# Optimization experiments

Measured on AMD Instinct MI355X. Metric: run time of the kernel, lower is better.

The kernel has to match this reference:

```python
import jax, jax.numpy as jnp
import numpy as np

VOCAB, EMB, SEQ, HID, TAGS, BATCH = 50000, 300, 256, 256, 50, 128


def _lstm_relu(x, Wx, Wh, b, reverse):
    """Keras LSTM with activation='relu', recurrent_activation='sigmoid'.
    x: [B,S,E] -> returns hidden states [B,S,H]. Gate order i,f,g,o (Keras)."""
    B = x.shape[0]
    H = Wh.shape[0]
    # Precompute input projections for all timesteps: [S,B,4H]
    xz = jnp.einsum('bse,eg->sbg', x, Wx) + b

    def step(carry, z_t):
        h, c = carry
        z = z_t + h @ Wh
        i, f, g, o = jnp.split(z, 4, axis=-1)
        c = jax.nn.sigmoid(f) * c + jax.nn.sigmoid(i) * jax.nn.relu(g)
        h = jax.nn.sigmoid(o) * jax.nn.relu(c)
        return (h, c), h

    h0 = jnp.zeros((B, H), x.dtype)
    _, hs = jax.lax.scan(step, (h0, h0), xz, reverse=reverse)  # hs: [S,B,H] in time order
    return jnp.swapaxes(hs, 0, 1)  # [B,S,H]


def setup_inputs() -> dict:
    key = jax.random.key(0)
    ks = jax.random.split(key, 10)
    s = 0.05  # small init keeps relu-LSTM states numerically tame
    return {
        'tokens': jax.random.randint(ks[0], (BATCH, SEQ), 0, VOCAB, dtype=jnp.int32),
        'emb':    jax.random.normal(ks[1], (VOCAB, EMB), jnp.float32) * s,
        'Wx_f':   jax.random.normal(ks[2], (EMB, 4 * HID), jnp.float32) * s,
        'Wh_f':   jax.random.normal(ks[3], (HID, 4 * HID), jnp.float32) * s,
        'b_f':    jnp.zeros((4 * HID,), jnp.float32),
        'Wx_b':   jax.random.normal(ks[4], (EMB, 4 * HID), jnp.float32) * s,
        'Wh_b':   jax.random.normal(ks[5], (HID, 4 * HID), jnp.float32) * s,
        'b_b':    jnp.zeros((4 * HID,), jnp.float32),
        'Wd':     jax.random.normal(ks[6], (2 * HID, TAGS), jnp.float32) * s,
        'bd':     jnp.zeros((TAGS,), jnp.float32),
    }


def reference(tokens, emb, Wx_f, Wh_f, b_f, Wx_b, Wh_b, b_b, Wd, bd):
    x = emb[tokens]                                  # [B,S,E] embedding lookup
    hf = _lstm_relu(x, Wx_f, Wh_f, b_f, reverse=False)
    hb = _lstm_relu(x, Wx_b, Wh_b, b_b, reverse=True)
    h = jnp.concatenate([hf, hb], axis=-1)           # [B,S,2H]
    # Dropout is identity at inference (Keras default training=False).
    return jax.nn.softmax(h @ Wd + bd, axis=-1)      # [B,S,TAGS]
```

## Files before the change

kernel.cpp:

```cpp
#include <hip/hip_runtime.h>
#include <stdint.h>

#define B_    128
#define S_    256
#define EMB_  300
#define HID_  256
#define TAGS_ 50
#define KPAD  320
#define NROWS (B_ * S_)
#define GF    (4 * HID_)
#define NCOLS (2 * GF)

typedef __bf16 bf16x8 __attribute__((ext_vector_type(8)));
typedef float  f32x4  __attribute__((ext_vector_type(4)));
typedef unsigned int u32x4 __attribute__((ext_vector_type(4)));
typedef int    i32x8  __attribute__((ext_vector_type(8)));

__device__ __forceinline__ unsigned short f2bf(float f) {
    unsigned int u = __float_as_uint(f);
    unsigned int r = (u + 0x7fffu + ((u >> 16) & 1u)) >> 16;
    return (unsigned short)r;
}
__device__ __forceinline__ bf16x8 ldb8(const unsigned short* p) {
    u32x4 v = *reinterpret_cast<const u32x4*>(p);
    return __builtin_bit_cast(bf16x8, v);
}
__device__ __forceinline__ float sigf(float x) {
    return __builtin_amdgcn_rcpf(1.0f + __builtin_amdgcn_exp2f(x * -1.44269504f));
}
__device__ __forceinline__ float sel2(f32x4 v, int p) {
    return p ? v[1] : v[0];
}
__device__ __forceinline__ void gload_lds16(const void* g, void* l) {
    __builtin_amdgcn_global_load_lds(
        (const __attribute__((address_space(1))) void*)g,
        (__attribute__((address_space(3))) void*)l, 16, 0, 0);
}

__global__ void k_gather_x(const int* __restrict__ tokens, const float* __restrict__ emb,
                           unsigned short* __restrict__ X16) {
    int r = blockIdx.x;
    int k = threadIdx.x;
    int b = r & 127, s = r >> 7;
    int tok = tokens[b * S_ + s];
    float v = (k < EMB_) ? emb[(long)tok * EMB_ + k] : 0.0f;
    X16[(long)r * KPAD + k] = f2bf(v);
}

__global__ void k_prep_w(const float* __restrict__ Wx_f, const float* __restrict__ Wx_b,
                         unsigned short* __restrict__ W16T) {
    int c = blockIdx.x;
    int k = threadIdx.x;
    float v = 0.0f;
    if (k < EMB_) v = (c < GF) ? Wx_f[k * GF + c] : Wx_b[k * GF + (c - GF)];
    W16T[c * KPAD + k] = f2bf(v);
}

__global__ void k_prep_wd(const float* __restrict__ Wd, unsigned short* __restrict__ WdT16) {
    int c = blockIdx.x;
    int k = threadIdx.x;
    float v = (c < TAGS_) ? Wd[k * TAGS_ + c] : 0.0f;
    WdT16[c * 512 + k] = f2bf(v);
}

__global__ void k_prep_wh8(const float* __restrict__ Wh_f, const float* __restrict__ Wh_b,
                           unsigned char* __restrict__ WhP8) {
    int row = blockIdx.x;
    int k = threadIdx.x;
    int d = row >> 10, rr = row & 1023, gi = rr >> 8, j = rr & 255;
    const float* Wh = d ? Wh_b : Wh_f;
    float v = Wh[k * GF + gi * HID_ + j];
    int p = __builtin_amdgcn_cvt_pk_fp8_f32(v, 0.0f, 0, false);
    WhP8[(long)row * 256 + k] = (unsigned char)(p & 0xff);
}

__global__ __launch_bounds__(256) void k_gemm_xz(
    const unsigned short* __restrict__ X16, const unsigned short* __restrict__ W16T,
    const float* __restrict__ b_f, const float* __restrict__ b_b,
    unsigned long long* __restrict__ xzP) {
    __shared__ __align__(16) unsigned short Asw[2][128 * 64];
    __shared__ __align__(16) unsigned short Bsw[2][128 * 64];
    int w = threadIdx.x >> 6, lane = threadIdx.x & 63;
    int quad = lane >> 4, l16 = lane & 15;
    int m0 = blockIdx.x * 128;
    int n0 = blockIdx.y * 128;

    int rlane = lane >> 3;
    int jpos  = lane & 7;
    int jsrc  = jpos ^ (rlane & 7);

    f32x4 acc[2][8];
#pragma unroll
    for (int mt = 0; mt < 2; ++mt)
#pragma unroll
        for (int nt = 0; nt < 8; ++nt) acc[mt][nt] = (f32x4){0.f, 0.f, 0.f, 0.f};

#define STAGE(ST, BUFI) do {                                                    \
    int k0_ = (ST) * 64;                                                        \
    _Pragma("unroll")                                                           \
    for (int i_ = 0; i_ < 4; ++i_) {                                            \
        int rb_ = (w * 4 + i_) * 8;                                             \
        int r_  = rb_ + rlane;                                                  \
        gload_lds16(X16 + (long)(m0 + r_) * KPAD + k0_ + jsrc * 8,              \
                    &Asw[BUFI][rb_ * 64]);                                      \
    }                                                                           \
    _Pragma("unroll")                                                           \
    for (int i_ = 0; i_ < 4; ++i_) {                                            \
        int rb_ = (w * 4 + i_) * 8;                                             \
        int r_  = rb_ + rlane;                                                  \
        gload_lds16(W16T + (long)(n0 + r_) * KPAD + k0_ + jsrc * 8,             \
                    &Bsw[BUFI][rb_ * 64]);                                      \
    }                                                                           \
} while (0)

    STAGE(0, 0);
    __syncthreads();
#pragma unroll
    for (int st = 0; st < 5; ++st) {
        if (st < 4) STAGE(st + 1, (st + 1) & 1);
        int bufi = st & 1;
#pragma unroll
        for (int ks = 0; ks < 2; ++ks) {
            bf16x8 a[2], bb[8];
#pragma unroll
            for (int mt = 0; mt < 2; ++mt) {
                int mrow = w * 32 + mt * 16 + l16;
                int jp = (ks * 4 + quad) ^ (l16 & 7);
                a[mt] = ldb8(&Asw[bufi][mrow * 64 + jp * 8]);
            }
#pragma unroll
            for (int nt = 0; nt < 8; ++nt) {
                int nrow = nt * 16 + l16;
                int jp = (ks * 4 + quad) ^ (l16 & 7);
                bb[nt] = ldb8(&Bsw[bufi][nrow * 64 + jp * 8]);
            }
#pragma unroll
            for (int mt = 0; mt < 2; ++mt)
#pragma unroll
                for (int nt = 0; nt < 8; ++nt)
                    acc[mt][nt] = __builtin_amdgcn_mfma_f32_16x16x32_bf16(a[mt], bb[nt], acc[mt][nt], 0, 0, 0);
        }
        __syncthreads();
    }
#undef STAGE

    int s = blockIdx.x;
#pragma unroll
    for (int mt = 0; mt < 2; ++mt) {
        int grp = w * 2 + mt;
#pragma unroll
        for (int nt = 0; nt < 8; ++nt) {
            int col = n0 + nt * 16 + l16;
            int dir = col >> 10, cc = col & 1023;
            int gate = cc >> 8, u16 = (cc & 255) >> 4;
            float bias = dir ? b_b[cc] : b_f[cc];
            unsigned long long pk = 0;
#pragma unroll
            for (int r = 0; r < 4; ++r)
                pk |= (unsigned long long)f2bf(acc[mt][nt][r] + bias) << (16 * r);
            long idx8 = ((long)(s * 16 + dir * 8 + grp)) * 4096 +
                        (gate * 16 + u16) * 64 + quad * 16 + l16;
            xzP[idx8] = pk;
        }
    }
}

__global__ __launch_bounds__(512, 2) void k_recurrence(
    const unsigned char* __restrict__ WhP8,
    const unsigned long long* __restrict__ xzP, unsigned short* __restrict__ hcat16) {
    __shared__ __align__(16) unsigned char lds[1152];
    int tid = threadIdx.x;
    int w = tid >> 6, lane = tid & 63, quad = lane >> 4, l16 = lane & 15;
    int blk = blockIdx.x;
    int d = blk >> 6, bg2 = blk & 63;
    int p = quad & 1;
    int cg = quad >> 1;
    int col = 16 * (2 * w + cg) + l16;
    int rp = l16 & 1;

    i32x8 wh8s[4][2][2];
#pragma unroll
    for (int gi = 0; gi < 4; ++gi)
#pragma unroll
        for (int cgi = 0; cgi < 2; ++cgi)
#pragma unroll
            for (int kt2 = 0; kt2 < 2; ++kt2) {
                const unsigned char* wp8 = WhP8 +
                    ((long)((d * 4 + gi) * 256 + 16 * (2 * w + cgi) + l16)) * 256 +
                    kt2 * 128 + quad * 32;
                i32x8 v = *reinterpret_cast<const i32x8*>(wp8);
                asm volatile("" : "+v"(v));
                wh8s[gi][cgi][kt2] = v;
            }

    float c2 = 0.f;

    const unsigned short* xzU = (const unsigned short*)xzP;
    int rowc = d * 8 + (bg2 >> 3);
    unsigned int laneoff = (unsigned)((2 * w + cg) * 256 +
                                      (((bg2 >> 1) & 3) * 16 + l16) * 4 +
                                      2 * (bg2 & 1) + p);

    unsigned short xzu[4];
    {
        int s0 = d ? 255 : 0;
        const unsigned short* ps = xzU + (unsigned long)(s0 * 16 + rowc) * 16384;
#pragma unroll
        for (int ga = 0; ga < 4; ++ga) xzu[ga] = ps[laneoff + ga * 4096];
    }

    for (int t = 0; t < 256; ++t) {
        int s = d ? (255 - t) : t;
        int pb = t & 1, cb = pb ^ 1;
        f32x4 acc8[4][2];
#pragma unroll
        for (int gi = 0; gi < 4; ++gi)
#pragma unroll
            for (int cgi = 0; cgi < 2; ++cgi) acc8[gi][cgi] = (f32x4){0.f, 0.f, 0.f, 0.f};

        if (t > 0) {
#pragma unroll
            for (int kt2 = 0; kt2 < 2; ++kt2) {
                i32x8 A8 = *reinterpret_cast<const i32x8*>(
                    lds + cb * 576 + rp * 288 + kt2 * 128 + quad * 32);
#pragma unroll
                for (int cgi = 0; cgi < 2; ++cgi)
#pragma unroll
                    for (int gi = 0; gi < 4; ++gi)
#if __has_builtin(__builtin_amdgcn_mfma_scale_f32_16x16x128_f8f6f4)
                        acc8[gi][cgi] = __builtin_amdgcn_mfma_scale_f32_16x16x128_f8f6f4(
                            A8, wh8s[gi][cgi][kt2], acc8[gi][cgi], 0, 0, 0, 0x7F, 0, 0x7F);
#else
                        acc8[gi][cgi] = acc8[gi][cgi];
#endif
            }
        }
        float xa0 = __uint_as_float((unsigned int)xzu[0] << 16);
        float xa1 = __uint_as_float((unsigned int)xzu[1] << 16);
        float xa2 = __uint_as_float((unsigned int)xzu[2] << 16);
        float xa3 = __uint_as_float((unsigned int)xzu[3] << 16);
        {
            int sn = d ? (s ? s - 1 : 0) : (s < 255 ? s + 1 : 255);
            const unsigned short* ps = xzU + (unsigned long)(sn * 16 + rowc) * 16384;
#pragma unroll
            for (int ga = 0; ga < 4; ++ga) xzu[ga] = ps[laneoff + ga * 4096];
        }
        float zi = (cg ? sel2(acc8[0][1], p) : sel2(acc8[0][0], p)) + xa0;
        float zf = (cg ? sel2(acc8[1][1], p) : sel2(acc8[1][0], p)) + xa1;
        float zg = (cg ? sel2(acc8[2][1], p) : sel2(acc8[2][0], p)) + xa2;
        float zo = (cg ? sel2(acc8[3][1], p) : sel2(acc8[3][0], p)) + xa3;
        float c = sigf(zf) * c2 + sigf(zi) * fmaxf(zg, 0.0f);
        c2 = c;
        float h = sigf(zo) * fmaxf(c, 0.0f);

        int p8 = __builtin_amdgcn_cvt_pk_fp8_f32(h, h, 0, false);
        *(lds + pb * 576 + p * 288 + col) = (unsigned char)(p8 & 0xff);
        hcat16[((long)(bg2 * 2 + p) * S_ + s) * 512 + d * HID_ + col] = f2bf(h);
        asm volatile("s_waitcnt lgkmcnt(0)\n\ts_barrier" ::: "memory");
    }
}

__global__ __launch_bounds__(256) void k_gemm_logits(
    const unsigned short* __restrict__ hcat16, const unsigned short* __restrict__ WdT16,
    const float* __restrict__ bd, float* __restrict__ out) {
    int w = threadIdx.x >> 6, lane = threadIdx.x & 63;
    int quad = lane >> 4, l16 = lane & 15;
    int m0 = blockIdx.x * 128 + w * 32;
    f32x4 acc[2][4];
#pragma unroll
    for (int mt = 0; mt < 2; ++mt)
#pragma unroll
        for (int nt = 0; nt < 4; ++nt) acc[mt][nt] = (f32x4){0.f, 0.f, 0.f, 0.f};
#pragma unroll
    for (int ks = 0; ks < 16; ++ks) {
        int k0 = ks * 32 + quad * 8;
        bf16x8 a[2], bb[4];
#pragma unroll
        for (int mt = 0; mt < 2; ++mt)
            a[mt] = ldb8(hcat16 + (long)(m0 + mt * 16 + l16) * 512 + k0);
#pragma unroll
        for (int nt = 0; nt < 4; ++nt)
            bb[nt] = ldb8(WdT16 + (long)(nt * 16 + l16) * 512 + k0);
#pragma unroll
        for (int mt = 0; mt < 2; ++mt)
#pragma unroll
            for (int nt = 0; nt < 4; ++nt)
                acc[mt][nt] = __builtin_amdgcn_mfma_f32_16x16x32_bf16(a[mt], bb[nt], acc[mt][nt], 0, 0, 0);
    }
#pragma unroll
    for (int mt = 0; mt < 2; ++mt) {
#pragma unroll
        for (int r = 0; r < 4; ++r) {
            int row = m0 + mt * 16 + quad * 4 + r;
            float vv[4];
            float mx = -3.0e38f;
#pragma unroll
            for (int nt = 0; nt < 4; ++nt) {
                int cl = nt * 16 + l16;
                float tv = (cl < TAGS_) ? (acc[mt][nt][r] + bd[cl]) : -3.0e38f;
                vv[nt] = tv;
                mx = fmaxf(mx, tv);
            }
#pragma unroll
            for (int off = 8; off >= 1; off >>= 1) mx = fmaxf(mx, __shfl_xor(mx, off, 64));
            float sum = 0.f;
#pragma unroll
            for (int nt = 0; nt < 4; ++nt) {
                int cl = nt * 16 + l16;
                float e = (cl < TAGS_) ? __expf(vv[nt] - mx) : 0.0f;
                vv[nt] = e;
                sum += e;
            }
#pragma unroll
            for (int off = 8; off >= 1; off >>= 1) sum += __shfl_xor(sum, off, 64);
            float rs = __builtin_amdgcn_rcpf(sum);
#pragma unroll
            for (int nt = 0; nt < 4; ++nt) {
                int cl = nt * 16 + l16;
                if (cl < TAGS_) out[(long)row * TAGS_ + cl] = vv[nt] * rs;
            }
        }
    }
}

extern "C" void kernel_launch(void* const* d_in, const int* in_sizes, int n_in,
                              void* d_out, int out_size, void* d_ws, size_t ws_size,
                              hipStream_t stream) {
    (void)in_sizes; (void)n_in; (void)out_size; (void)ws_size;
    const int*   tokens = (const int*)  d_in[0];
    const float* emb    = (const float*)d_in[1];
    const float* Wx_f   = (const float*)d_in[2];
    const float* Wh_f   = (const float*)d_in[3];
    const float* b_f    = (const float*)d_in[4];
    const float* Wx_b   = (const float*)d_in[5];
    const float* Wh_b   = (const float*)d_in[6];
    const float* b_b    = (const float*)d_in[7];
    const float* Wd     = (const float*)d_in[8];
    const float* bd     = (const float*)d_in[9];
    float* out = (float*)d_out;

    uint8_t* w = (uint8_t*)d_ws;
    unsigned short* X16    = (unsigned short*)(w);
    unsigned char*  WhP8   = (unsigned char*)(w);
    unsigned short* W16T   = (unsigned short*)(w + 20971520);
    unsigned short* WdT16  = (unsigned short*)(w + 22282240);
    unsigned long long* xzP = (unsigned long long*)(w + 22347776);
    unsigned short* hcat16 = (unsigned short*)(w + 156565504);

    k_gather_x  <<<dim3(NROWS),     dim3(KPAD), 0, stream>>>(tokens, emb, X16);
    k_prep_w    <<<dim3(NCOLS),     dim3(KPAD), 0, stream>>>(Wx_f, Wx_b, W16T);
    k_prep_wd   <<<dim3(64),        dim3(512),  0, stream>>>(Wd, WdT16);
    k_gemm_xz   <<<dim3(256, 16),   dim3(256),  0, stream>>>(X16, W16T, b_f, b_b, xzP);
    k_prep_wh8  <<<dim3(2048),      dim3(256),  0, stream>>>(Wh_f, Wh_b, WhP8);
    k_recurrence<<<dim3(128),       dim3(512),  0, stream>>>(WhP8, xzP, hcat16);
    k_gemm_logits<<<dim3(256),      dim3(256),  0, stream>>>(hcat16, WdT16, bd, out);
}
```

Measured before the change: 423.0 us.

## Merge prep kernels and stage logits GEMM operands through double-buffered swizzled LDS

The three small prep kernels (embedding gather, Wx transpose, Wd transpose) become one launch that dispatches on block index, which removes two kernel launches. The logits GEMM now loads hcat16 and WdT16 tiles into XOR-swizzled shared memory with async global_load_lds and a double buffer, so the next K-stage load overlaps the current MFMAs. Before, each wave read its operands straight from global memory. The change adds LDS use and barriers, and the logits kernel is likely a small share of total time next to the recurrence.

```diff
diff --git a/kernel.cpp b/kernel.cpp
--- a/kernel.cpp
+++ b/kernel.cpp
@@ -37,30 +37,31 @@
         (__attribute__((address_space(3))) void*)l, 16, 0, 0);
 }
 
-__global__ void k_gather_x(const int* __restrict__ tokens, const float* __restrict__ emb,
-                           unsigned short* __restrict__ X16) {
-    int r = blockIdx.x;
-    int k = threadIdx.x;
-    int b = r & 127, s = r >> 7;
-    int tok = tokens[b * S_ + s];
-    float v = (k < EMB_) ? emb[(long)tok * EMB_ + k] : 0.0f;
-    X16[(long)r * KPAD + k] = f2bf(v);
-}
-
-__global__ void k_prep_w(const float* __restrict__ Wx_f, const float* __restrict__ Wx_b,
-                         unsigned short* __restrict__ W16T) {
-    int c = blockIdx.x;
-    int k = threadIdx.x;
-    float v = 0.0f;
-    if (k < EMB_) v = (c < GF) ? Wx_f[k * GF + c] : Wx_b[k * GF + (c - GF)];
-    W16T[c * KPAD + k] = f2bf(v);
-}
-
-__global__ void k_prep_wd(const float* __restrict__ Wd, unsigned short* __restrict__ WdT16) {
-    int c = blockIdx.x;
-    int k = threadIdx.x;
-    float v = (c < TAGS_) ? Wd[k * TAGS_ + c] : 0.0f;
-    WdT16[c * 512 + k] = f2bf(v);
+__global__ void k_prep_all(const int* __restrict__ tokens, const float* __restrict__ emb,
+                           const float* __restrict__ Wx_f, const float* __restrict__ Wx_b,
+                           const float* __restrict__ Wd,
+                           unsigned short* __restrict__ X16,
+                           unsigned short* __restrict__ W16T,
+                           unsigned short* __restrict__ WdT16) {
+    int blk = blockIdx.x, k = threadIdx.x;
+    if (blk < NROWS) {
+        int b = blk & 127, s = blk >> 7;
+        int tok = tokens[b * S_ + s];
+        float v = (k < EMB_) ? emb[(long)tok * EMB_ + k] : 0.0f;
+        X16[(long)blk * KPAD + k] = f2bf(v);
+    } else if (blk < NROWS + NCOLS) {
+        int c = blk - NROWS;
+        float v = 0.0f;
+        if (k < EMB_) v = (c < GF) ? Wx_f[k * GF + c] : Wx_b[k * GF + (c - GF)];
+        W16T[c * KPAD + k] = f2bf(v);
+    } else {
+        int e = (blk - NROWS - NCOLS) * 320 + k;
+        if (e < 64 * 512) {
+            int c = e >> 9, kk = e & 511;
+            float v = (c < TAGS_) ? Wd[kk * TAGS_ + c] : 0.0f;
+            WdT16[c * 512 + kk] = f2bf(v);
+        }
+    }
 }
 
 __global__ void k_prep_wh8(const float* __restrict__ Wh_f, const float* __restrict__ Wh_b,
@@ -263,35 +264,74 @@
 __global__ __launch_bounds__(256) void k_gemm_logits(
     const unsigned short* __restrict__ hcat16, const unsigned short* __restrict__ WdT16,
     const float* __restrict__ bd, float* __restrict__ out) {
+    __shared__ __align__(16) unsigned short Asw[2][128 * 64];
+    __shared__ __align__(16) unsigned short Bsw[2][64 * 64];
     int w = threadIdx.x >> 6, lane = threadIdx.x & 63;
     int quad = lane >> 4, l16 = lane & 15;
-    int m0 = blockIdx.x * 128 + w * 32;
+    int m0 = blockIdx.x * 128;
+    int rlane = lane >> 3, jpos = lane & 7;
+    int jsrc = jpos ^ (rlane & 7);
+
     f32x4 acc[2][4];
 #pragma unroll
     for (int mt = 0; mt < 2; ++mt)
 #pragma unroll
         for (int nt = 0; nt < 4; ++nt) acc[mt][nt] = (f32x4){0.f, 0.f, 0.f, 0.f};
-#pragma unroll
-    for (int ks = 0; ks < 16; ++ks) {
-        int k0 = ks * 32 + quad * 8;
-        bf16x8 a[2], bb[4];
-#pragma unroll
-        for (int mt = 0; mt < 2; ++mt)
-            a[mt] = ldb8(hcat16 + (long)(m0 + mt * 16 + l16) * 512 + k0);
-#pragma unroll
-        for (int nt = 0; nt < 4; ++nt)
-            bb[nt] = ldb8(WdT16 + (long)(nt * 16 + l16) * 512 + k0);
-#pragma unroll
-        for (int mt = 0; mt < 2; ++mt)
-#pragma unroll
-            for (int nt = 0; nt < 4; ++nt)
-                acc[mt][nt] = __builtin_amdgcn_mfma_f32_16x16x32_bf16(a[mt], bb[nt], acc[mt][nt], 0, 0, 0);
-    }
+
+#define STAGE3(ST, BUFI) do {                                                   \
+    int k0_ = (ST) * 64;                                                        \
+    _Pragma("unroll")                                                           \
+    for (int i_ = 0; i_ < 4; ++i_) {                                            \
+        int rb_ = (w * 4 + i_) * 8;                                             \
+        int r_  = rb_ + rlane;                                                  \
+        gload_lds16(hcat16 + (long)(m0 + r_) * 512 + k0_ + jsrc * 8,            \
+                    &Asw[BUFI][rb_ * 64]);                                      \
+    }                                                                           \
+    _Pragma("unroll")                                                           \
+    for (int i_ = 0; i_ < 2; ++i_) {                                            \
+        int rb_ = (w * 2 + i_) * 8;                                             \
+        int r_  = rb_ + rlane;                                                  \
+        gload_lds16(WdT16 + (long)r_ * 512 + k0_ + jsrc * 8,                    \
+                    &Bsw[BUFI][rb_ * 64]);                                      \
+    }                                                                           \
+} while (0)
+
+    STAGE3(0, 0);
+    __syncthreads();
+#pragma unroll
+    for (int st = 0; st < 8; ++st) {
+        if (st < 7) STAGE3(st + 1, (st + 1) & 1);
+        int bufi = st & 1;
+#pragma unroll
+        for (int ks = 0; ks < 2; ++ks) {
+            bf16x8 a[2], bb[4];
+#pragma unroll
+            for (int mt = 0; mt < 2; ++mt) {
+                int mrow = w * 32 + mt * 16 + l16;
+                int jp = (ks * 4 + quad) ^ (l16 & 7);
+                a[mt] = ldb8(&Asw[bufi][mrow * 64 + jp * 8]);
+            }
+#pragma unroll
+            for (int nt = 0; nt < 4; ++nt) {
+                int nrow = nt * 16 + l16;
+                int jp = (ks * 4 + quad) ^ (l16 & 7);
+                bb[nt] = ldb8(&Bsw[bufi][nrow * 64 + jp * 8]);
+            }
+#pragma unroll
+            for (int mt = 0; mt < 2; ++mt)
+#pragma unroll
+                for (int nt = 0; nt < 4; ++nt)
+                    acc[mt][nt] = __builtin_amdgcn_mfma_f32_16x16x32_bf16(a[mt], bb[nt], acc[mt][nt], 0, 0, 0);
+        }
+        __syncthreads();
+    }
+#undef STAGE3
+
 #pragma unroll
     for (int mt = 0; mt < 2; ++mt) {
 #pragma unroll
         for (int r = 0; r < 4; ++r) {
-            int row = m0 + mt * 16 + quad * 4 + r;
+            int row = m0 + w * 32 + mt * 16 + quad * 4 + r;
             float vv[4];
             float mx = -3.0e38f;
 #pragma unroll
@@ -347,9 +387,8 @@
     unsigned long long* xzP = (unsigned long long*)(w + 22347776);
     unsigned short* hcat16 = (unsigned short*)(w + 156565504);
 
-    k_gather_x  <<<dim3(NROWS),     dim3(KPAD), 0, stream>>>(tokens, emb, X16);
-    k_prep_w    <<<dim3(NCOLS),     dim3(KPAD), 0, stream>>>(Wx_f, Wx_b, W16T);
-    k_prep_wd   <<<dim3(64),        dim3(512),  0, stream>>>(Wd, WdT16);
+    k_prep_all  <<<dim3(NROWS + NCOLS + 103), dim3(KPAD), 0, stream>>>(
+        tokens, emb, Wx_f, Wx_b, Wd, X16, W16T, WdT16);
     k_gemm_xz   <<<dim3(256, 16),   dim3(256),  0, stream>>>(X16, W16T, b_f, b_b, xzP);
     k_prep_wh8  <<<dim3(2048),      dim3(256),  0, stream>>>(Wh_f, Wh_b, WhP8);
     k_recurrence<<<dim3(128),       dim3(512),  0, stream>>>(WhP8, xzP, hcat16);
```

Result: faster. 412.9 us (-2.4%).
